# Performance work log

Hardware: AMD Instinct MI355X
Metric: run time of the kernel (lower is better)

Reference implementation:

```python
import jax, jax.numpy as jnp
import numpy as np

DIM = 2048
N_HEADS = 32
N_KV = 8
HEAD_DIM = DIM // N_HEADS  # 64
N_REP = N_HEADS // N_KV    # 4
HALF = HEAD_DIM // 2
B = 2
T = 2048
THETA = 10000.0


def _rope(x, cos, sin):
    # x: [B,H,T,hd]; cos/sin: [T,HALF]. Pairs are interleaved (..., half, 2),
    # matching torch.view_as_complex on a (..., -1, 2) reshape.
    xr = x.reshape(x.shape[:-1] + (HALF, 2))
    x0, x1 = xr[..., 0], xr[..., 1]
    o0 = x0 * cos - x1 * sin
    o1 = x0 * sin + x1 * cos
    return jnp.stack([o0, o1], axis=-1).reshape(x.shape)


def setup_inputs() -> dict:
    key = jax.random.key(0)
    ks = jax.random.split(key, 6)
    x = jax.random.normal(ks[0], (B, T, DIM), dtype=jnp.float32)
    scale = 0.02
    wq = jax.random.normal(ks[1], (N_HEADS * HEAD_DIM, DIM), dtype=jnp.float32) * scale
    wk = jax.random.normal(ks[2], (N_KV * HEAD_DIM, DIM), dtype=jnp.float32) * scale
    wv = jax.random.normal(ks[3], (N_KV * HEAD_DIM, DIM), dtype=jnp.float32) * scale
    wo = jax.random.normal(ks[4], (DIM, DIM), dtype=jnp.float32) * scale
    # causal mask [1,1,T,T]
    mask = jnp.tril(jnp.ones((T, T), dtype=jnp.int32))[None, None]
    # RoPE tables (precompute_freqs_cis with theta=10000, scaling_factor=1.0)
    freqs = 1.0 / THETA ** (jnp.arange(HALF, dtype=jnp.float32) / HALF)
    angles = jnp.arange(2 * T, dtype=jnp.float32)[:, None] * freqs[None, :]
    return {"x": x, "mask": mask, "wq": wq, "wk": wk, "wv": wv, "wo": wo,
            "cos": jnp.cos(angles), "sin": jnp.sin(angles)}


def reference(x, mask, wq, wk, wv, wo, cos, sin):
    Bx, Tx, C = x.shape
    q = (x @ wq.T).reshape(Bx, Tx, N_HEADS, HEAD_DIM).transpose(0, 2, 1, 3)
    k = (x @ wk.T).reshape(Bx, Tx, N_KV, HEAD_DIM).transpose(0, 2, 1, 3)
    v = (x @ wv.T).reshape(Bx, Tx, N_KV, HEAD_DIM).transpose(0, 2, 1, 3)
    q = _rope(q, cos[:Tx], sin[:Tx])
    k = _rope(k, cos[:Tx], sin[:Tx])
    # GQA: head h attends to kv head h // N_REP (repeat_interleave semantics)
    qg = q.reshape(Bx, N_KV, N_REP, Tx, HEAD_DIM)
    att = jnp.einsum('bgrtd,bgsd->bgrts', qg, k) * (HEAD_DIM ** -0.5)
    m = mask[0, 0, :Tx, :Tx]  # broadcast over b,g,r
    att = jnp.where(m == 0, -jnp.inf, att)
    att = jax.nn.softmax(att, axis=-1)
    og = jnp.einsum('bgrts,bgsd->bgrtd', att, v)
    out = og.reshape(Bx, N_HEADS, Tx, HEAD_DIM).transpose(0, 2, 1, 3).reshape(Bx, Tx, C)
    return out @ wo.T
```

## Files before the change

kernel.cpp:

```cpp
#include <hip/hip_runtime.h>
#include <hip/hip_bf16.h>

typedef unsigned short u16;
typedef __attribute__((ext_vector_type(8))) short s16x8;
typedef __attribute__((ext_vector_type(4))) float f32x4;
typedef __attribute__((ext_vector_type(16))) float f32x16;
typedef __attribute__((ext_vector_type(4))) float f32x4v;
typedef __attribute__((ext_vector_type(4))) u16 u16x4;

#define DIM 2048
#define NH 32
#define NKV 8
#define HD 64
#define TT 2048
#define BB 2
#define MT (BB * TT)

__device__ __forceinline__ u16 f2bf(float f) {
    union { float f; unsigned u; } v; v.f = f;
    unsigned r = v.u + 0x7FFFu + ((v.u >> 16) & 1u);
    return (u16)(r >> 16);
}
__device__ __forceinline__ float bf2f(u16 h) {
    union { unsigned u; float f; } v; v.u = ((unsigned)h) << 16;
    return v.f;
}
__device__ __forceinline__ u16 cvtbf(float f) {
    __hip_bfloat16 hb = __float2bfloat16(f);
    return *reinterpret_cast<u16*>(&hb);
}
__device__ __forceinline__ void plane32swap(unsigned& a, unsigned& b) {
#if defined(__has_builtin)
#if __has_builtin(__builtin_amdgcn_permlane32_swap)
    auto t = __builtin_amdgcn_permlane32_swap((int)a, (int)b, false, false);
    a = (unsigned)t[0]; b = (unsigned)t[1];
#else
    asm volatile("v_permlane32_swap_b32 %0, %1" : "+v"(a), "+v"(b));
#endif
#else
    asm volatile("v_permlane32_swap_b32 %0, %1" : "+v"(a), "+v"(b));
#endif
}

__global__ void k_convert(const float* __restrict__ src, u16* __restrict__ dst, int n) {
    int i = (blockIdx.x * 256 + threadIdx.x) * 4;
    if (i >= n) return;
    f32x4v f = *(const f32x4v*)(src + i);
    u16x4 o;
    #pragma unroll
    for (int e = 0; e < 4; ++e) o[e] = f2bf(f[e]);
    *(u16x4*)(dst + i) = o;
}

template<bool OUTF32>
__global__ __launch_bounds__(512, 2) void k_gemm256(const u16* __restrict__ A, const u16* __restrict__ B,
                                                    void* __restrict__ C, int M, int N, int K) {
    __shared__ u16 LDS[65536];
    const int nTn = N >> 8;
    const int nwg = gridDim.x;
    const int wg = (blockIdx.x & 7) * (nwg >> 3) + (blockIdx.x >> 3);
    const int tm = wg / nTn, tn = wg % nTn;
    const int tid = threadIdx.x, wid = tid >> 6, lane = tid & 63;
    const int wr = wid >> 2, wc = wid & 3;
    const u16* Ab = A + (size_t)tm * 256 * K;
    const u16* Bb = B + (size_t)tn * 256 * K;

    f32x4 acc[8][4] = {};
    s16x8 af[4], bfr[4];

    auto STAGE = [&](int isB, int buf, int kk, int kt) {
        u16* base = LDS + (isB ? 32768 : 0) + (buf * 2 + kk) * 8192;
        const u16* g = (isB ? Bb : Ab) + kt * 64 + kk * 32;
        #pragma unroll
        for (int i = 0; i < 2; ++i) {
            const int s = i * 512 + tid;
            const int row = s >> 2;
            const int cl = (s & 3) ^ ((row >> 1) & 3);
            __builtin_amdgcn_global_load_lds(
                (const __attribute__((address_space(1))) void*)(g + (size_t)row * K + cl * 8),
                (__attribute__((address_space(3))) void*)(base + (i * 512 + wid * 64) * 8), 16, 0, 0);
        }
    };
    auto LDA = [&](int buf, int kk, int mh) {
        const u16* base = LDS + (buf * 2 + kk) * 8192;
        #pragma unroll
        for (int m2 = 0; m2 < 4; ++m2) {
            const int row = wr * 128 + (mh * 4 + m2) * 16 + (lane & 15);
            const int cl = (lane >> 4) ^ ((row >> 1) & 3);
            af[m2] = *(const s16x8*)(base + row * 32 + cl * 8);
        }
    };
    auto LDB = [&](int buf, int kk) {
        const u16* base = LDS + 32768 + (buf * 2 + kk) * 8192;
        #pragma unroll
        for (int n = 0; n < 4; ++n) {
            const int row = wc * 64 + n * 16 + (lane & 15);
            const int cl = (lane >> 4) ^ ((row >> 1) & 3);
            bfr[n] = *(const s16x8*)(base + row * 32 + cl * 8);
        }
    };
    auto MFMA16 = [&](int mh) {
        asm volatile("s_waitcnt lgkmcnt(0)" ::: "memory");
        __builtin_amdgcn_sched_barrier(0);
        __builtin_amdgcn_s_setprio(1);
        #pragma unroll
        for (int m2 = 0; m2 < 4; ++m2)
            #pragma unroll
            for (int n = 0; n < 4; ++n)
                acc[mh * 4 + m2][n] =
                    __builtin_amdgcn_mfma_f32_16x16x32_bf16(af[m2], bfr[n], acc[mh * 4 + m2][n], 0, 0, 0);
        __builtin_amdgcn_s_setprio(0);
    };

    STAGE(0, 0, 0, 0); STAGE(1, 0, 0, 0);
    STAGE(0, 0, 1, 0); STAGE(1, 0, 1, 0);
    STAGE(0, 1, 0, 1); STAGE(1, 1, 0, 1);
    asm volatile("s_waitcnt vmcnt(8)" ::: "memory");
    __builtin_amdgcn_s_barrier();

    const int NI = K >> 7;
    for (int it = 0; it < NI; ++it) {
        const bool last = (it == NI - 1);
        const int t1 = 2 * it + 1;
        LDA(0, 0, 0); LDB(0, 0);
        STAGE(0, 1, 1, t1);
        __builtin_amdgcn_s_barrier();
        MFMA16(0);
        __builtin_amdgcn_s_barrier();
        LDA(0, 0, 1);
        STAGE(1, 1, 1, t1);
        __builtin_amdgcn_s_barrier();
        MFMA16(1);
        asm volatile("s_waitcnt vmcnt(8)" ::: "memory");
        __builtin_amdgcn_s_barrier();
        LDA(0, 1, 0); LDB(0, 1);
        if (!last) STAGE(0, 0, 0, t1 + 1);
        __builtin_amdgcn_s_barrier();
        MFMA16(0);
        __builtin_amdgcn_s_barrier();
        LDA(0, 1, 1);
        if (!last) STAGE(1, 0, 0, t1 + 1);
        __builtin_amdgcn_s_barrier();
        MFMA16(1);
        if (!last) asm volatile("s_waitcnt vmcnt(8)" ::: "memory");
        else       asm volatile("s_waitcnt vmcnt(4)" ::: "memory");
        __builtin_amdgcn_s_barrier();
        LDA(1, 0, 0); LDB(1, 0);
        if (!last) STAGE(0, 0, 1, t1 + 1);
        __builtin_amdgcn_s_barrier();
        MFMA16(0);
        __builtin_amdgcn_s_barrier();
        LDA(1, 0, 1);
        if (!last) STAGE(1, 0, 1, t1 + 1);
        __builtin_amdgcn_s_barrier();
        MFMA16(1);
        if (!last) asm volatile("s_waitcnt vmcnt(8)" ::: "memory");
        else       asm volatile("s_waitcnt vmcnt(0)" ::: "memory");
        __builtin_amdgcn_s_barrier();
        LDA(1, 1, 0); LDB(1, 1);
        if (!last) STAGE(0, 1, 0, t1 + 2);
        __builtin_amdgcn_s_barrier();
        MFMA16(0);
        __builtin_amdgcn_s_barrier();
        LDA(1, 1, 1);
        if (!last) STAGE(1, 1, 0, t1 + 2);
        __builtin_amdgcn_s_barrier();
        MFMA16(1);
        if (!last) {
            asm volatile("s_waitcnt vmcnt(8)" ::: "memory");
        }
        __builtin_amdgcn_s_barrier();
    }

    #pragma unroll
    for (int mf = 0; mf < 8; ++mf)
        #pragma unroll
        for (int n = 0; n < 4; ++n)
            #pragma unroll
            for (int r = 0; r < 4; ++r) {
                const int row = tm * 256 + wr * 128 + mf * 16 + (lane >> 4) * 4 + r;
                const int col = tn * 256 + wc * 64 + n * 16 + (lane & 15);
                if (OUTF32) ((float*)C)[(size_t)row * N + col] = acc[mf][n][r];
                else        ((u16*)C)[(size_t)row * N + col] = f2bf(acc[mf][n][r]);
            }
}

__global__ void k_rope(const u16* __restrict__ qkv, const float* __restrict__ ct, const float* __restrict__ st,
                       u16* __restrict__ qo, u16* __restrict__ ko, u16* __restrict__ vo) {
    const int idx = blockIdx.x * 256 + threadIdx.x;
    const int c = idx % 384;
    const int bt = idx / 384;
    const int b = bt / TT, t = bt % TT;
    const s16x8 v = *(const s16x8*)(qkv + (size_t)bt * 3072 + c * 8);
    if (c < 320) {
        const bool isq = c < 256;
        const int base = isq ? c : c - 256;
        const int hh = base >> 3;
        const int di0 = (base & 7) * 4;
        const f32x4v cc = *(const f32x4v*)(ct + t * 32 + di0);
        const f32x4v ss = *(const f32x4v*)(st + t * 32 + di0);
        const float QS = isq ? 0.18033688f : 1.0f;
        s16x8 o;
        #pragma unroll
        for (int p = 0; p < 4; ++p) {
            const float x0 = bf2f((u16)v[2 * p]), x1 = bf2f((u16)v[2 * p + 1]);
            o[2 * p]     = (short)cvtbf((x0 * cc[p] - x1 * ss[p]) * QS);
            o[2 * p + 1] = (short)cvtbf((x0 * ss[p] + x1 * cc[p]) * QS);
        }
        u16* dst = isq ? (qo + ((size_t)(b * NH + hh) * TT + t) * HD + 2 * di0)
                       : (ko + ((size_t)(b * NKV + hh) * TT + t) * HD + 2 * di0);
        *(s16x8*)dst = o;
    } else {
        const int base = c - 320;
        const int hh = base >> 3;
        const int d0 = (base & 7) * 8;
        *(s16x8*)(vo + ((size_t)(b * NKV + hh) * TT + t) * HD + d0) = v;
    }
}

__global__ __launch_bounds__(256) void k_vtrans(const u16* __restrict__ vp, u16* __restrict__ vt) {
    __shared__ u16 tile[64][66];
    const int bg = blockIdx.x >> 5;
    const int t0 = (blockIdx.x & 31) * 64;
    const int tid = threadIdx.x;
    #pragma unroll
    for (int c = 0; c < 2; ++c) {
        const int idx = c * 256 + tid;
        const int tl = idx >> 3, dc = idx & 7;
        s16x8 v = *(const s16x8*)(vp + ((size_t)bg * TT + t0 + tl) * HD + dc * 8);
        *(s16x8*)(&tile[tl][dc * 8]) = v;
    }
    __syncthreads();
    #pragma unroll
    for (int c = 0; c < 2; ++c) {
        const int idx = c * 256 + tid;
        const int d = idx >> 3, tc = idx & 7;
        s16x8 v;
        #pragma unroll
        for (int e = 0; e < 8; ++e) v[e] = (short)tile[tc * 8 + e][d];
        *(s16x8*)(vt + ((size_t)bg * HD + d) * TT + t0 + tc * 8) = v;
    }
}

__global__ __launch_bounds__(256) void k_attn(const u16* __restrict__ Q, const u16* __restrict__ K,
                                              const u16* __restrict__ Vtg, u16* __restrict__ O) {
    const int bid = blockIdx.x;
    const int qt = 15 - (bid >> 6);
    const int bh = bid & 63;
    const int h = bh & 31;
    const int b = bh >> 5;
    const int g = h >> 2;
    __shared__ u16 Ks[3][64 * 64];
    __shared__ u16 Vs[3][64 * 64];
    const int tid = threadIdx.x, wave = tid >> 6, lane = tid & 63;
    const int c = lane & 31, hi = lane >> 5;
    const u16* Qg = Q + ((size_t)(b * NH + h) * TT + qt * 128) * HD;
    const u16* Kg = K + (size_t)(b * NKV + g) * TT * HD;
    const u16* Vg = Vtg + (size_t)(b * NKV + g) * HD * TT;

    s16x8 qa[4];
    #pragma unroll
    for (int kb = 0; kb < 4; ++kb)
        qa[kb] = *(const s16x8*)(Qg + (size_t)(wave * 32 + c) * HD + kb * 16 + hi * 8);

    const int rl = lane >> 3, ccl = lane & 7;
    auto stage = [&](int jj, int bi) {
        u16* Kb = Ks[bi];
        u16* Vb = Vs[bi];
        #pragma unroll
        for (int cc = 0; cc < 2; ++cc) {
            const int r = wave * 16 + cc * 8 + rl;
            const int sc = ccl ^ (r & 7);
            __builtin_amdgcn_global_load_lds(
                (const __attribute__((address_space(1))) void*)(Kg + ((size_t)(jj * 64 + r)) * HD + sc * 8),
                (__attribute__((address_space(3))) void*)(Kb + (wave * 16 + cc * 8) * 64), 16, 0, 0);
            __builtin_amdgcn_global_load_lds(
                (const __attribute__((address_space(1))) void*)(Vg + (size_t)r * TT + jj * 64 + sc * 8),
                (__attribute__((address_space(3))) void*)(Vb + (wave * 16 + cc * 8) * 64), 16, 0, 0);
        }
    };

    f32x16 acc0 = {}, acc1 = {};
    float l = 0.f;
    const int ntiles = 2 * qt + 2;

    stage(0, 0);
    stage(1, 1);

    for (int j = 0; j < ntiles; ++j) {
        if (j < ntiles - 1) asm volatile("s_waitcnt vmcnt(4)" ::: "memory");
        else                asm volatile("s_waitcnt vmcnt(0)" ::: "memory");
        __builtin_amdgcn_s_barrier();
        if (j + 2 < ntiles) stage(j + 2, (j + 2) % 3);
        const int bi = j % 3;
        const u16* Kb = Ks[bi];
        const u16* Vb = Vs[bi];

        f32x16 s0 = {}, s1 = {};
        __builtin_amdgcn_s_setprio(1);
        #pragma unroll
        for (int kb = 0; kb < 4; ++kb) {
            const s16x8 kf0 = *(const s16x8*)(Kb + c * 64 + (((2 * kb + hi) ^ ccl) * 8));
            const s16x8 kf1 = *(const s16x8*)(Kb + (32 + c) * 64 + (((2 * kb + hi) ^ ccl) * 8));
            s0 = __builtin_amdgcn_mfma_f32_32x32x16_bf16(kf0, qa[kb], s0, 0, 0, 0);
            s1 = __builtin_amdgcn_mfma_f32_32x32x16_bf16(kf1, qa[kb], s1, 0, 0, 0);
        }
        __builtin_amdgcn_s_setprio(0);

        if (j >= ntiles - 2) {
            const int q_loc = wave * 32 + c;
            const int kb64 = (j - (ntiles - 2)) * 64;
            #pragma unroll
            for (int r = 0; r < 16; ++r) {
                const int crow = (r & 3) + 8 * (r >> 2) + 4 * hi;
                if (kb64 + crow > q_loc)      s0[r] = -1e30f;
                if (kb64 + 32 + crow > q_loc) s1[r] = -1e30f;
            }
        }
        #pragma unroll
        for (int r = 0; r < 16; ++r) {
            s0[r] = __builtin_amdgcn_exp2f(s0[r]); l += s0[r];
            s1[r] = __builtin_amdgcn_exp2f(s1[r]); l += s1[r];
        }

        unsigned W0[8], W1[8];
        #pragma unroll
        for (int m = 0; m < 8; ++m) {
            float a0f = s0[2 * m], a1f = s0[2 * m + 1];
            float b0f = s1[2 * m], b1f = s1[2 * m + 1];
            asm("v_cvt_pk_bf16_f32 %0, %1, %2" : "=v"(W0[m]) : "v"(a0f), "v"(a1f));
            asm("v_cvt_pk_bf16_f32 %0, %1, %2" : "=v"(W1[m]) : "v"(b0f), "v"(b1f));
        }
        s16x8 pa[4];
        #pragma unroll
        for (int ks = 0; ks < 4; ++ks) {
            const int base = 4 * (ks & 1);
            unsigned a0 = (ks < 2) ? W0[base + 0] : W1[base + 0];
            unsigned b0 = (ks < 2) ? W0[base + 2] : W1[base + 2];
            unsigned a1 = (ks < 2) ? W0[base + 1] : W1[base + 1];
            unsigned b1 = (ks < 2) ? W0[base + 3] : W1[base + 3];
            plane32swap(a0, b0);
            plane32swap(a1, b1);
            union { unsigned w[4]; s16x8 v; } u;
            u.w[0] = a0; u.w[1] = a1; u.w[2] = b0; u.w[3] = b1;
            pa[ks] = u.v;
        }

        __builtin_amdgcn_s_setprio(1);
        #pragma unroll
        for (int kb = 0; kb < 4; ++kb) {
            const s16x8 vb0 = *(const s16x8*)(Vb + c * 64 + (((2 * kb + hi) ^ ccl) * 8));
            const s16x8 vb1 = *(const s16x8*)(Vb + (32 + c) * 64 + (((2 * kb + hi) ^ ccl) * 8));
            acc0 = __builtin_amdgcn_mfma_f32_32x32x16_bf16(pa[kb], vb0, acc0, 0, 0, 0);
            acc1 = __builtin_amdgcn_mfma_f32_32x32x16_bf16(pa[kb], vb1, acc1, 0, 0, 0);
        }
        __builtin_amdgcn_s_setprio(0);
    }

    l += __shfl_xor(l, 32, 64);
    const float inv = 1.0f / l;
    #pragma unroll
    for (int r = 0; r < 16; ++r) {
        const int crow = (r & 3) + 8 * (r >> 2) + 4 * hi;
        const float li = __shfl(inv, crow, 64);
        const size_t row = (size_t)b * TT + qt * 128 + wave * 32 + crow;
        O[row * DIM + h * 64 + c]      = cvtbf(acc0[r] * li);
        O[row * DIM + h * 64 + 32 + c] = cvtbf(acc1[r] * li);
    }
}

extern "C" void kernel_launch(void* const* d_in, const int* in_sizes, int n_in,
                              void* d_out, int out_size, void* d_ws, size_t ws_size,
                              hipStream_t stream) {
    const float* x  = (const float*)d_in[0];
    const float* wq = (const float*)d_in[2];
    const float* wk = (const float*)d_in[3];
    const float* wv = (const float*)d_in[4];
    const float* wo = (const float*)d_in[5];
    const float* ct = (const float*)d_in[6];
    const float* st = (const float*)d_in[7];
    char* ws = (char*)d_ws;
    u16* xb   = (u16*)(ws);
    u16* wqkv = (u16*)(ws + 16777216);
    u16* wob  = (u16*)(ws + 29360128);
    u16* qkv  = (u16*)(ws + 37748736);
    u16* kr   = (u16*)(ws + 62914560);
    u16* vp   = (u16*)(ws + 67108864);
    u16* qr   = xb;
    u16* ao   = qkv;
    u16* vt   = wqkv;

    k_convert<<<MT * DIM / 1024, 256, 0, stream>>>(x, xb, MT * DIM);
    k_convert<<<DIM * DIM / 1024, 256, 0, stream>>>(wq, wqkv, DIM * DIM);
    k_convert<<<512 * DIM / 1024, 256, 0, stream>>>(wk, wqkv + (size_t)DIM * DIM, 512 * DIM);
    k_convert<<<512 * DIM / 1024, 256, 0, stream>>>(wv, wqkv + (size_t)DIM * DIM + (size_t)512 * DIM, 512 * DIM);
    k_convert<<<DIM * DIM / 1024, 256, 0, stream>>>(wo, wob, DIM * DIM);

    k_gemm256<false><<<(MT / 256) * (3072 / 256), 512, 0, stream>>>(xb, wqkv, qkv, MT, 3072, DIM);
    k_rope<<<MT * 384 / 256, 256, 0, stream>>>(qkv, ct, st, qr, kr, vp);
    k_vtrans<<<BB * NKV * (TT / 64), 256, 0, stream>>>(vp, vt);
    k_attn<<<16 * 64, 256, 0, stream>>>(qr, kr, vt, ao);
    k_gemm256<true><<<(MT / 256) * (DIM / 256), 512, 0, stream>>>(ao, wob, d_out, MT, DIM, DIM);
}
```

Measured before the change: 194.9 us.

## Fuse conversions, narrow GEMM N-tiles, and restructure attention K/V LDS layout

Merges the five fp32-to-bf16 conversion launches into a single kernel that dispatches on a flat index, saving launch overhead. The GEMM kernel is templated on the N-tile width: 256x192 tiles for the QKV projection and 256x128 for the output projection. This raises the workgroup count to fill the CUs better, at the cost of less reuse per tile. The attention kernel changes its K/V global-to-LDS staging to a contiguous 8x8-chunk layout with new fragment read offsets, replacing the XOR swizzle.

```diff
diff --git a/kernel.cpp b/kernel.cpp
--- a/kernel.cpp
+++ b/kernel.cpp
@@ -42,35 +42,45 @@
 #endif
 }
 
-__global__ void k_convert(const float* __restrict__ src, u16* __restrict__ dst, int n) {
-    int i = (blockIdx.x * 256 + threadIdx.x) * 4;
-    if (i >= n) return;
-    f32x4v f = *(const f32x4v*)(src + i);
-    u16x4 o;
-    #pragma unroll
-    for (int e = 0; e < 4; ++e) o[e] = f2bf(f[e]);
-    *(u16x4*)(dst + i) = o;
-}
-
-template<bool OUTF32>
+__global__ void k_convert_all(const float* __restrict__ x, const float* __restrict__ wq,
+                              const float* __restrict__ wk, const float* __restrict__ wv,
+                              const float* __restrict__ wo,
+                              u16* __restrict__ xb, u16* __restrict__ wqkv, u16* __restrict__ wob) {
+    long i = (long)(blockIdx.x * 256 + threadIdx.x) * 4;
+    const float* src; u16* dst; long o = i;
+    if (o < 8388608L)            { src = x;  dst = xb; }
+    else if ((o -= 8388608L) < 4194304L) { src = wq; dst = wqkv; }
+    else if ((o -= 4194304L) < 1048576L) { src = wk; dst = wqkv + 4194304L; }
+    else if ((o -= 1048576L) < 1048576L) { src = wv; dst = wqkv + 5242880L; }
+    else { o -= 1048576L;          src = wo; dst = wob; }
+    f32x4v f = *(const f32x4v*)(src + o);
+    u16x4 out;
+    #pragma unroll
+    for (int e = 0; e < 4; ++e) out[e] = f2bf(f[e]);
+    *(u16x4*)(dst + o) = out;
+}
+
+template<int BNF, bool OUTF32>
 __global__ __launch_bounds__(512, 2) void k_gemm256(const u16* __restrict__ A, const u16* __restrict__ B,
                                                     void* __restrict__ C, int M, int N, int K) {
-    __shared__ u16 LDS[65536];
-    const int nTn = N >> 8;
+    constexpr int BN = 64 * BNF;
+    constexpr int BH = 2048 * BNF;
+    __shared__ u16 LDS[32768 + 4 * BH];
+    const int nTn = N / BN;
     const int nwg = gridDim.x;
     const int wg = (blockIdx.x & 7) * (nwg >> 3) + (blockIdx.x >> 3);
     const int tm = wg / nTn, tn = wg % nTn;
     const int tid = threadIdx.x, wid = tid >> 6, lane = tid & 63;
     const int wr = wid >> 2, wc = wid & 3;
     const u16* Ab = A + (size_t)tm * 256 * K;
-    const u16* Bb = B + (size_t)tn * 256 * K;
-
-    f32x4 acc[8][4] = {};
-    s16x8 af[4], bfr[4];
-
-    auto STAGE = [&](int isB, int buf, int kk, int kt) {
-        u16* base = LDS + (isB ? 32768 : 0) + (buf * 2 + kk) * 8192;
-        const u16* g = (isB ? Bb : Ab) + kt * 64 + kk * 32;
+    const u16* Bb = B + (size_t)tn * BN * K;
+
+    f32x4 acc[8][BNF] = {};
+    s16x8 af[4], bfr[BNF];
+
+    auto STAGE_A = [&](int buf, int kk, int kt) {
+        u16* base = LDS + (buf * 2 + kk) * 8192;
+        const u16* g = Ab + kt * 64 + kk * 32;
         #pragma unroll
         for (int i = 0; i < 2; ++i) {
             const int s = i * 512 + tid;
@@ -81,6 +91,20 @@
                 (__attribute__((address_space(3))) void*)(base + (i * 512 + wid * 64) * 8), 16, 0, 0);
         }
     };
+    auto STAGE_B = [&](int buf, int kk, int kt) {
+        u16* base = LDS + 32768 + (buf * 2 + kk) * BH;
+        const u16* g = Bb + kt * 64 + kk * 32;
+        auto one = [&](int ch) {
+            const int row = ch * 16 + (lane >> 2);
+            const int cl = (lane & 3) ^ ((row >> 1) & 3);
+            __builtin_amdgcn_global_load_lds(
+                (const __attribute__((address_space(1))) void*)(g + (size_t)row * K + cl * 8),
+                (__attribute__((address_space(3))) void*)(base + ch * 512), 16, 0, 0);
+        };
+        if constexpr (BNF == 4) { one(wid); one(8 + wid); }
+        else if constexpr (BNF == 3) { one(wid); one(8 + (wid & 3)); }
+        else { one(wid); }
+    };
     auto LDA = [&](int buf, int kk, int mh) {
         const u16* base = LDS + (buf * 2 + kk) * 8192;
         #pragma unroll
@@ -91,10 +115,10 @@
         }
     };
     auto LDB = [&](int buf, int kk) {
-        const u16* base = LDS + 32768 + (buf * 2 + kk) * 8192;
-        #pragma unroll
-        for (int n = 0; n < 4; ++n) {
-            const int row = wc * 64 + n * 16 + (lane & 15);
+        const u16* base = LDS + 32768 + (buf * 2 + kk) * BH;
+        #pragma unroll
+        for (int n = 0; n < BNF; ++n) {
+            const int row = wc * (16 * BNF) + n * 16 + (lane & 15);
             const int cl = (lane >> 4) ^ ((row >> 1) & 3);
             bfr[n] = *(const s16x8*)(base + row * 32 + cl * 8);
         }
@@ -106,16 +130,21 @@
         #pragma unroll
         for (int m2 = 0; m2 < 4; ++m2)
             #pragma unroll
-            for (int n = 0; n < 4; ++n)
+            for (int n = 0; n < BNF; ++n)
                 acc[mh * 4 + m2][n] =
                     __builtin_amdgcn_mfma_f32_16x16x32_bf16(af[m2], bfr[n], acc[mh * 4 + m2][n], 0, 0, 0);
         __builtin_amdgcn_s_setprio(0);
     };
 
-    STAGE(0, 0, 0, 0); STAGE(1, 0, 0, 0);
-    STAGE(0, 0, 1, 0); STAGE(1, 0, 1, 0);
-    STAGE(0, 1, 0, 1); STAGE(1, 1, 0, 1);
-    asm volatile("s_waitcnt vmcnt(8)" ::: "memory");
+    #define VMID() do { if constexpr (BNF == 2) asm volatile("s_waitcnt vmcnt(6)" ::: "memory"); \
+                        else                    asm volatile("s_waitcnt vmcnt(8)" ::: "memory"); } while (0)
+    #define VONE() do { if constexpr (BNF == 2) asm volatile("s_waitcnt vmcnt(3)" ::: "memory"); \
+                        else                    asm volatile("s_waitcnt vmcnt(4)" ::: "memory"); } while (0)
+
+    STAGE_A(0, 0, 0); STAGE_B(0, 0, 0);
+    STAGE_A(0, 1, 0); STAGE_B(0, 1, 0);
+    STAGE_A(1, 0, 1); STAGE_B(1, 0, 1);
+    VMID();
     __builtin_amdgcn_s_barrier();
 
     const int NI = K >> 7;
@@ -123,63 +152,68 @@
         const bool last = (it == NI - 1);
         const int t1 = 2 * it + 1;
         LDA(0, 0, 0); LDB(0, 0);
-        STAGE(0, 1, 1, t1);
+        STAGE_A(1, 1, t1);
         __builtin_amdgcn_s_barrier();
         MFMA16(0);
         __builtin_amdgcn_s_barrier();
+
         LDA(0, 0, 1);
-        STAGE(1, 1, 1, t1);
+        STAGE_B(1, 1, t1);
         __builtin_amdgcn_s_barrier();
         MFMA16(1);
-        asm volatile("s_waitcnt vmcnt(8)" ::: "memory");
-        __builtin_amdgcn_s_barrier();
+        VMID();
+        __builtin_amdgcn_s_barrier();
+
         LDA(0, 1, 0); LDB(0, 1);
-        if (!last) STAGE(0, 0, 0, t1 + 1);
+        if (!last) STAGE_A(0, 0, t1 + 1);
         __builtin_amdgcn_s_barrier();
         MFMA16(0);
         __builtin_amdgcn_s_barrier();
+
         LDA(0, 1, 1);
-        if (!last) STAGE(1, 0, 0, t1 + 1);
+        if (!last) STAGE_B(0, 0, t1 + 1);
         __builtin_amdgcn_s_barrier();
         MFMA16(1);
-        if (!last) asm volatile("s_waitcnt vmcnt(8)" ::: "memory");
-        else       asm volatile("s_waitcnt vmcnt(4)" ::: "memory");
-        __builtin_amdgcn_s_barrier();
+        if (!last) VMID(); else VONE();
+        __builtin_amdgcn_s_barrier();
+
         LDA(1, 0, 0); LDB(1, 0);
-        if (!last) STAGE(0, 0, 1, t1 + 1);
+        if (!last) STAGE_A(0, 1, t1 + 1);
         __builtin_amdgcn_s_barrier();
         MFMA16(0);
         __builtin_amdgcn_s_barrier();
+
         LDA(1, 0, 1);
-        if (!last) STAGE(1, 0, 1, t1 + 1);
+        if (!last) STAGE_B(0, 1, t1 + 1);
         __builtin_amdgcn_s_barrier();
         MFMA16(1);
-        if (!last) asm volatile("s_waitcnt vmcnt(8)" ::: "memory");
-        else       asm volatile("s_waitcnt vmcnt(0)" ::: "memory");
-        __builtin_amdgcn_s_barrier();
+        if (!last) VMID(); else asm volatile("s_waitcnt vmcnt(0)" ::: "memory");
+        __builtin_amdgcn_s_barrier();
+
         LDA(1, 1, 0); LDB(1, 1);
-        if (!last) STAGE(0, 1, 0, t1 + 2);
+        if (!last) STAGE_A(1, 0, t1 + 2);
         __builtin_amdgcn_s_barrier();
         MFMA16(0);
         __builtin_amdgcn_s_barrier();
+
         LDA(1, 1, 1);
-        if (!last) STAGE(1, 1, 0, t1 + 2);
+        if (!last) STAGE_B(1, 0, t1 + 2);
         __builtin_amdgcn_s_barrier();
         MFMA16(1);
-        if (!last) {
-            asm volatile("s_waitcnt vmcnt(8)" ::: "memory");
-        }
-        __builtin_amdgcn_s_barrier();
-    }
+        if (!last) VMID();
+        __builtin_amdgcn_s_barrier();
+    }
+    #undef VMID
+    #undef VONE
 
     #pragma unroll
     for (int mf = 0; mf < 8; ++mf)
         #pragma unroll
-        for (int n = 0; n < 4; ++n)
+        for (int n = 0; n < BNF; ++n)
             #pragma unroll
             for (int r = 0; r < 4; ++r) {
                 const int row = tm * 256 + wr * 128 + mf * 16 + (lane >> 4) * 4 + r;
-                const int col = tn * 256 + wc * 64 + n * 16 + (lane & 15);
+                const int col = tn * BN + wc * (16 * BNF) + n * 16 + (lane & 15);
                 if (OUTF32) ((float*)C)[(size_t)row * N + col] = acc[mf][n][r];
                 else        ((u16*)C)[(size_t)row * N + col] = f2bf(acc[mf][n][r]);
             }
@@ -250,8 +284,8 @@
     const int h = bh & 31;
     const int b = bh >> 5;
     const int g = h >> 2;
-    __shared__ u16 Ks[3][64 * 64];
-    __shared__ u16 Vs[3][64 * 64];
+    __shared__ u16 Ks[3][4096];
+    __shared__ u16 Vs[3][4096];
     const int tid = threadIdx.x, wave = tid >> 6, lane = tid & 63;
     const int c = lane & 31, hi = lane >> 5;
     const u16* Qg = Q + ((size_t)(b * NH + h) * TT + qt * 128) * HD;
@@ -263,26 +297,27 @@
     for (int kb = 0; kb < 4; ++kb)
         qa[kb] = *(const s16x8*)(Qg + (size_t)(wave * 32 + c) * HD + kb * 16 + hi * 8);
 
-    const int rl = lane >> 3, ccl = lane & 7;
+    const int klo = (lane & 7) * HD + (lane >> 3) * 8;
+    const int vlo = (lane & 7) * TT + (lane >> 3) * 8;
     auto stage = [&](int jj, int bi) {
         u16* Kb = Ks[bi];
         u16* Vb = Vs[bi];
         #pragma unroll
-        for (int cc = 0; cc < 2; ++cc) {
-            const int r = wave * 16 + cc * 8 + rl;
-            const int sc = ccl ^ (r & 7);
+        for (int u2 = 0; u2 < 2; ++u2) {
+            const int u = wave * 2 + u2;
             __builtin_amdgcn_global_load_lds(
-                (const __attribute__((address_space(1))) void*)(Kg + ((size_t)(jj * 64 + r)) * HD + sc * 8),
-                (__attribute__((address_space(3))) void*)(Kb + (wave * 16 + cc * 8) * 64), 16, 0, 0);
+                (const __attribute__((address_space(1))) void*)(Kg + (size_t)jj * 4096 + u * 512 + klo),
+                (__attribute__((address_space(3))) void*)(Kb + u * 512), 16, 0, 0);
             __builtin_amdgcn_global_load_lds(
-                (const __attribute__((address_space(1))) void*)(Vg + (size_t)r * TT + jj * 64 + sc * 8),
-                (__attribute__((address_space(3))) void*)(Vb + (wave * 16 + cc * 8) * 64), 16, 0, 0);
+                (const __attribute__((address_space(1))) void*)(Vg + (size_t)u * 8 * TT + jj * 64 + vlo),
+                (__attribute__((address_space(3))) void*)(Vb + u * 512), 16, 0, 0);
         }
     };
 
     f32x16 acc0 = {}, acc1 = {};
     float l = 0.f;
     const int ntiles = 2 * qt + 2;
+    const int rbk = (c >> 3) * 512 + (c & 7) * 8 + hi * 64;
 
     stage(0, 0);
     stage(1, 1);
@@ -300,8 +335,8 @@
         __builtin_amdgcn_s_setprio(1);
         #pragma unroll
         for (int kb = 0; kb < 4; ++kb) {
-            const s16x8 kf0 = *(const s16x8*)(Kb + c * 64 + (((2 * kb + hi) ^ ccl) * 8));
-            const s16x8 kf1 = *(const s16x8*)(Kb + (32 + c) * 64 + (((2 * kb + hi) ^ ccl) * 8));
+            const s16x8 kf0 = *(const s16x8*)(Kb + rbk + kb * 128);
+            const s16x8 kf1 = *(const s16x8*)(Kb + rbk + kb * 128 + 2048);
             s0 = __builtin_amdgcn_mfma_f32_32x32x16_bf16(kf0, qa[kb], s0, 0, 0, 0);
             s1 = __builtin_amdgcn_mfma_f32_32x32x16_bf16(kf1, qa[kb], s1, 0, 0, 0);
         }
@@ -349,8 +384,8 @@
         __builtin_amdgcn_s_setprio(1);
         #pragma unroll
         for (int kb = 0; kb < 4; ++kb) {
-            const s16x8 vb0 = *(const s16x8*)(Vb + c * 64 + (((2 * kb + hi) ^ ccl) * 8));
-            const s16x8 vb1 = *(const s16x8*)(Vb + (32 + c) * 64 + (((2 * kb + hi) ^ ccl) * 8));
+            const s16x8 vb0 = *(const s16x8*)(Vb + rbk + kb * 128);
+            const s16x8 vb1 = *(const s16x8*)(Vb + rbk + kb * 128 + 2048);
             acc0 = __builtin_amdgcn_mfma_f32_32x32x16_bf16(pa[kb], vb0, acc0, 0, 0, 0);
             acc1 = __builtin_amdgcn_mfma_f32_32x32x16_bf16(pa[kb], vb1, acc1, 0, 0, 0);
         }
@@ -390,15 +425,11 @@
     u16* ao   = qkv;
     u16* vt   = wqkv;
 
-    k_convert<<<MT * DIM / 1024, 256, 0, stream>>>(x, xb, MT * DIM);
-    k_convert<<<DIM * DIM / 1024, 256, 0, stream>>>(wq, wqkv, DIM * DIM);
-    k_convert<<<512 * DIM / 1024, 256, 0, stream>>>(wk, wqkv + (size_t)DIM * DIM, 512 * DIM);
-    k_convert<<<512 * DIM / 1024, 256, 0, stream>>>(wv, wqkv + (size_t)DIM * DIM + (size_t)512 * DIM, 512 * DIM);
-    k_convert<<<DIM * DIM / 1024, 256, 0, stream>>>(wo, wob, DIM * DIM);
-
-    k_gemm256<false><<<(MT / 256) * (3072 / 256), 512, 0, stream>>>(xb, wqkv, qkv, MT, 3072, DIM);
+    k_convert_all<<<18432, 256, 0, stream>>>(x, wq, wk, wv, wo, xb, wqkv, wob);
+
+    k_gemm256<3, false><<<(MT / 256) * (3072 / 192), 512, 0, stream>>>(xb, wqkv, qkv, MT, 3072, DIM);
     k_rope<<<MT * 384 / 256, 256, 0, stream>>>(qkv, ct, st, qr, kr, vp);
     k_vtrans<<<BB * NKV * (TT / 64), 256, 0, stream>>>(vp, vt);
     k_attn<<<16 * 64, 256, 0, stream>>>(qr, kr, vt, ao);
-    k_gemm256<true><<<(MT / 256) * (DIM / 256), 512, 0, stream>>>(ao, wob, d_out, MT, DIM, DIM);
-}
+    k_gemm256<2, true><<<(MT / 256) * (DIM / 128), 512, 0, stream>>>(ao, wob, d_out, MT, DIM, DIM);
+}
```

New measurement: 176.1 us. 9.6% less time.
